# Kernel tuning notes

Measured on AMD Instinct MI355X. Metric: run time of the kernel, lower is better.

## Reference

```python
import jax, jax.numpy as jnp
import numpy as np

EPS = float(jnp.finfo(jnp.float32).eps)


def _mlp(x, W1, b1, W2, b2, W3, b3):
    h = jax.nn.relu(x @ W1 + b1)
    h = jax.nn.relu(h @ W2 + b2)
    return h @ W3 + b3


def setup_inputs() -> dict:
    B, D_A, D_B, K, H = 131072, 16, 16, 32, 256
    key = jax.random.key(0)
    ks = jax.random.split(key, 13)
    def lin(k, fi, fo):
        return jax.random.normal(k, (fi, fo), jnp.float32) * (fi ** -0.5)
    inp = {
        "x": jax.random.uniform(ks[0], (B, D_A + D_B), jnp.float32),
        "hW1": lin(ks[1], D_A, H), "hb1": jnp.zeros((H,), jnp.float32),
        "hW2": lin(ks[2], H, H),   "hb2": jnp.zeros((H,), jnp.float32),
        "hW3": lin(ks[3], H, D_B * (K + 1)), "hb3": jnp.zeros((D_B * (K + 1),), jnp.float32),
        "wW1": lin(ks[4], D_A, H), "wb1": jnp.zeros((H,), jnp.float32),
        "wW2": lin(ks[5], H, H),   "wb2": jnp.zeros((H,), jnp.float32),
        "wW3": lin(ks[6], H, D_B * K), "wb3": jnp.zeros((D_B * K,), jnp.float32),
        "A_dims": jnp.arange(0, 32, 2, dtype=jnp.int32),
        "B_dims": jnp.arange(1, 32, 2, dtype=jnp.int32),
    }
    return inp


def reference(x, hW1, hb1, hW2, hb2, hW3, hb3, wW1, wb1, wW2, wb2, wW3, wb3, A_dims, B_dims):
    B = x.shape[0]
    D_B = B_dims.shape[0]
    K = wW3.shape[1] // D_B
    x_A = x[:, A_dims]               # (B, D_A)
    x_B = x[:, B_dims]               # (B, D_B)

    raw_h = _mlp(x_A, hW1, hb1, hW2, hb2, hW3, hb3).reshape(B, D_B, K + 1)
    heights = jax.nn.softplus(raw_h) + EPS
    raw_w = _mlp(x_A, wW1, wb1, wW2, wb2, wW3, wb3).reshape(B, D_B, K)
    widths = jax.nn.softmax(raw_w, axis=-1)
    zeros = jnp.zeros((B, D_B, 1), x.dtype)
    bins = jnp.concatenate([zeros, jnp.cumsum(widths, axis=-1)], axis=-1)  # (B, D_B, K+1)

    # preprocess_params_2: normalise PDF heights and bin areas
    bin_widths = bins[:, :, 1:] - bins[:, :, :-1]
    bin_areas = 0.5 * (heights[:, :, :-1] + heights[:, :, 1:]) * bin_widths  # (B, D_B, K)
    total_area = bin_areas.sum(axis=-1, keepdims=True)
    v = heights / total_area
    bin_areas = bin_areas / total_area

    # bin search
    i = jnp.sum(x_B[..., None] >= bins, axis=-1) - 1
    i = jnp.clip(i, 0, K - 1)                                  # (B, D_B)
    iu = i[..., None]

    x_left = jnp.take_along_axis(bins, iu, axis=2)[..., 0]
    x_right = jnp.take_along_axis(bins, iu + 1, axis=2)[..., 0]
    w_b = x_right - x_left
    v_left = jnp.take_along_axis(v, iu, axis=2)[..., 0]
    v_right = jnp.take_along_axis(v, iu + 1, axis=2)[..., 0]
    w_v = v_right - v_left

    alpha = (x_B - x_left) / (w_b + EPS)
    # cumulative area up to left edge of bin i: exclusive prefix sum then gather
    c_edges = jnp.concatenate([zeros, jnp.cumsum(bin_areas, axis=-1)], axis=-1)
    c_left = jnp.take_along_axis(c_edges, iu, axis=2)[..., 0]

    y_B = c_left + 0.5 * alpha ** 2 * w_v * w_b + alpha * v_left * w_b
    y = x.at[:, B_dims].set(y_B)
    return y
```

## Files before the change

### kernel.cpp

```cpp
#include <hip/hip_runtime.h>
#include <cmath>

typedef short short8 __attribute__((ext_vector_type(8)));
typedef short short4v __attribute__((ext_vector_type(4)));
typedef float f32x16 __attribute__((ext_vector_type(16)));

#define EPSF 1.1920929e-07f

#define LDS_A2W 0
#define LDS_A2H 16896
#define LDS_A1W 33792
#define LDS_A1H 50688
#define LDS_EW  33792
#define LDS_HH  52224
#define LDS_XA  70656
#define LDS_TOTAL 71680

#define OFF1H 0
#define OFF1W 4096
#define OFF2H 8192
#define OFF2W 73728
#define OFF3H 139264
#define OFF3W 278528

__device__ __forceinline__ unsigned short f2bf(float f) {
  union { float f; unsigned u; } v; v.f = f;
  return (unsigned short)((v.u + 0x8000u) >> 16);
}
__device__ __forceinline__ float bf2f(unsigned short h) {
  union { unsigned u; float f; } v; v.u = ((unsigned)h) << 16; return v.f;
}

__global__ void pack_weights(const float* __restrict__ hW1, const float* __restrict__ wW1,
                             const float* __restrict__ hW2, const float* __restrict__ wW2,
                             const float* __restrict__ hW3, const float* __restrict__ wW3,
                             unsigned short* __restrict__ out) {
  int tile = blockIdx.x, l = threadIdx.x;
  const float* src; unsigned short* dst; int NT, N, K, base;
  if (tile < 8)        { src = hW1; dst = out + OFF1H; NT = 8;  N = 256; K = 16;  base = tile; }
  else if (tile < 16)  { src = wW1; dst = out + OFF1W; NT = 8;  N = 256; K = 16;  base = tile - 8; }
  else if (tile < 144) { src = hW2; dst = out + OFF2H; NT = 8;  N = 256; K = 256; base = tile - 16; }
  else if (tile < 272) { src = wW2; dst = out + OFF2W; NT = 8;  N = 256; K = 256; base = tile - 144; }
  else if (tile < 544) { src = hW3; dst = out + OFF3H; NT = 17; N = 528; K = 256; base = tile - 272; }
  else                 { src = wW3; dst = out + OFF3W; NT = 16; N = 512; K = 256; base = tile - 544; }
  int nt = base % NT, kt = base / NT, KTT = K / 16;
  int n = nt * 32 + (l & 31);
  int k0 = kt * 16 + (l >> 5) * 8;
  short8 v;
  #pragma unroll
  for (int e = 0; e < 8; e++) {
    float f = (n < N && (k0 + e) < K) ? src[(k0 + e) * N + n] : 0.f;
    v[e] = (short)f2bf(f);
  }
  int idx = nt * KTT + kt;
  *(short8*)(dst + (idx * 64 + l) * 8) = v;
}

template <int KT>
__device__ __forceinline__ f32x16 gemm_tile(const unsigned short* __restrict__ A, int apitch,
                                            const unsigned short* __restrict__ pB, int ct,
                                            float init) {
  int l = threadIdx.x & 63;
  f32x16 acc;
  #pragma unroll
  for (int r = 0; r < 16; r++) acc[r] = init;
  const unsigned short* aptr = A + (l & 31) * apitch + (l >> 5) * 8;
  const unsigned short* bptr = pB + (ct * KT * 64 + l) * 8;
  #pragma unroll
  for (int kt = 0; kt < KT; kt++) {
    short8 b = *(const short8*)(bptr + kt * 512);
    short8 a = *(const short8*)(aptr + kt * 16);
    acc = __builtin_amdgcn_mfma_f32_32x32x16_bf16(a, b, acc, 0, 0, 0);
  }
  return acc;
}

__device__ __forceinline__ void epi_relu(char* lds, int oOff, f32x16 acc, int ct) {
  int l = threadIdx.x & 63;
  int col = ct * 32 + (l & 31);
  unsigned short* o = (unsigned short*)(lds + oOff) + col + 4 * (l >> 5) * 264;
  #pragma unroll
  for (int r = 0; r < 16; r++) {
    int row = (r & 3) + 8 * (r >> 2);
    o[row * 264] = f2bf(fmaxf(acc[r], 0.f));
  }
}

__global__ __launch_bounds__(512, 4) void fused_kernel(
    const float* __restrict__ x,
    const float* __restrict__ hb1, const float* __restrict__ hb2, const float* __restrict__ hb3,
    const float* __restrict__ wb1, const float* __restrict__ wb2, const float* __restrict__ wb3,
    const unsigned short* __restrict__ pw,
    float* __restrict__ y) {
  extern __shared__ char lds[];
  const int t = threadIdx.x;
  const int w = t >> 6, l = t & 63;
  const int r0 = blockIdx.x * 32;

  if (t < 256) {
    int row = t >> 3, c4 = t & 7;
    float4 v = *(const float4*)(x + (r0 + row) * 32 + c4 * 4);
    y[(r0 + row) * 32 + c4 * 4] = v.x;
    y[(r0 + row) * 32 + c4 * 4 + 2] = v.z;
    unsigned short* xa = (unsigned short*)(lds + LDS_XA) + row * 16 + c4 * 2;
    xa[0] = f2bf(v.x); xa[1] = f2bf(v.z);
  }
  __syncthreads();

  const unsigned short* XA  = (const unsigned short*)(lds + LDS_XA);
  const unsigned short* A1W = (const unsigned short*)(lds + LDS_A1W);
  const unsigned short* A1H = (const unsigned short*)(lds + LDS_A1H);
  const unsigned short* A2W = (const unsigned short*)(lds + LDS_A2W);
  const unsigned short* A2H = (const unsigned short*)(lds + LDS_A2H);
  const int colw = w * 32 + (l & 31);

  { f32x16 aw = gemm_tile<1>(XA, 16, pw + OFF1W, w, wb1[colw]);
    epi_relu(lds, LDS_A1W, aw, w);
    f32x16 ah = gemm_tile<1>(XA, 16, pw + OFF1H, w, hb1[colw]);
    epi_relu(lds, LDS_A1H, ah, w); }
  __syncthreads();
  { f32x16 aw = gemm_tile<16>(A1W, 264, pw + OFF2W, w, wb2[colw]);
    epi_relu(lds, LDS_A2W, aw, w);
    f32x16 ah = gemm_tile<16>(A1H, 264, pw + OFF2H, w, hb2[colw]);
    epi_relu(lds, LDS_A2H, ah, w); }
  __syncthreads();

  #pragma unroll 1
  for (int H = 0; H < 2; H++) {
    for (int u = w; u < 17; u += 8) {
      int rbase = 4 * (l >> 5);
      if (u < 8) {
        int ctg = H * 8 + u;
        f32x16 a = gemm_tile<16>(A2W, 264, pw + OFF3W, ctg, wb3[ctg * 32 + (l & 31)]);
        unsigned short* o = (unsigned short*)(lds + LDS_EW) + rbase * 288 + (ctg & 7) * 36 + (l & 31);
        #pragma unroll
        for (int r = 0; r < 16; r++) {
          int row = (r & 3) + 8 * (r >> 2);
          o[row * 288] = f2bf(__expf(a[r]));
        }
      } else {
        int ctg = (u - 8) + 8 * H;
        int c = ctg * 32 + (l & 31);
        float bv = (c < 528) ? hb3[c] : 0.f;
        f32x16 a = gemm_tile<16>(A2H, 264, pw + OFF3H, ctg, bv);
        if (c >= 264 * H && c < 264 * (H + 1)) {
          unsigned d = ((unsigned)c * 993u) >> 15;
          int j = c - 33 * (int)d;
          unsigned short* o = (unsigned short*)(lds + LDS_HH) + rbase * 288 + ((int)d & 7) * 36 + j;
          #pragma unroll
          for (int r = 0; r < 16; r++) {
            int row = (r & 3) + 8 * (r >> 2);
            float v = a[r];
            float sp = fmaxf(v, 0.f) + __logf(1.f + __expf(-fabsf(v))) + EPSF;
            o[row * 288] = f2bf(sp);
          }
        }
      }
    }
    __syncthreads();

    {
      int p = t >> 1, half = t & 1;
      int row = p >> 3, dl = p & 7, dg = H * 8 + dl;
      const unsigned short* EWb = (const unsigned short*)(lds + LDS_EW) + row * 288 + dl * 36;
      const unsigned short* HHb = (const unsigned short*)(lds + LDS_HH) + row * 288 + dl * 36;
      const unsigned short* EWp = EWb + half * 16;
      const unsigned short* HHp = HHb + half * 16;
      float e[16], hh[17];
      #pragma unroll
      for (int i = 0; i < 4; i++) {
        short4v ev = *(const short4v*)(EWp + i * 4);
        short4v hv = *(const short4v*)(HHp + i * 4);
        #pragma unroll
        for (int jj = 0; jj < 4; jj++) {
          e[i * 4 + jj] = bf2f((unsigned short)ev[jj]);
          hh[i * 4 + jj] = bf2f((unsigned short)hv[jj]);
        }
      }
      hh[16] = bf2f(HHp[16]);
      float se = 0.f;
      #pragma unroll
      for (int k = 0; k < 16; k++) se += e[k];
      float so = __shfl_xor(se, 1);
      float s = se + so;
      float xbv = x[(r0 + row) * 32 + 2 * dg + 1];
      float xbs = xbv * s;
      float bl0 = half ? so : 0.f;
      int fnd = (xbs >= bl0) ? 1 : 0;
      float bl = bl0, cl2 = 0.f, sxl = bl0, scl2 = 0.f;
      int ki = 0;
      #pragma unroll
      for (int k = 0; k < 16; k++) {
        bool c = (xbs >= bl);
        ki   = c ? k   : ki;
        sxl  = c ? bl  : sxl;
        scl2 = c ? cl2 : scl2;
        cl2 += (hh[k] + hh[k + 1]) * e[k];
        bl  += e[k];
      }
      float cl2o = __shfl_xor(cl2, 1);
      float S2 = cl2 + cl2o;
      if (half) scl2 += cl2o;
      int   o_ki   = __shfl_xor(ki, 1);
      float o_sxl  = __shfl_xor(sxl, 1);
      float o_scl2 = __shfl_xor(scl2, 1);
      int   o_fnd  = __shfl_xor(fnd, 1);
      bool other = half ? (fnd == 0) : (o_fnd != 0);
      int   gki   = other ? o_ki   : ki;
      int   ghalf = other ? (half ^ 1) : half;
      float gsxl  = other ? o_sxl  : sxl;
      float gscl2 = other ? o_scl2 : scl2;
      int go = ghalf * 16 + gki;
      float sew = bf2f(EWb[go]);
      float shl = bf2f(HHb[go]);
      float shr = bf2f(HHb[go + 1]);
      float alpha = (xbs - gsxl) / (sew + EPSF);
      float yv = (gscl2 + (alpha * alpha * (shr - shl) + 2.f * alpha * shl) * sew) / S2;
      if (!half) y[(r0 + row) * 32 + 2 * dg + 1] = yv;
    }
    __syncthreads();
  }
}

extern "C" void kernel_launch(void* const* d_in, const int* in_sizes, int n_in,
                              void* d_out, int out_size, void* d_ws, size_t ws_size,
                              hipStream_t stream) {
  const float* x   = (const float*)d_in[0];
  const float* hW1 = (const float*)d_in[1];
  const float* hb1 = (const float*)d_in[2];
  const float* hW2 = (const float*)d_in[3];
  const float* hb2 = (const float*)d_in[4];
  const float* hW3 = (const float*)d_in[5];
  const float* hb3 = (const float*)d_in[6];
  const float* wW1 = (const float*)d_in[7];
  const float* wb1 = (const float*)d_in[8];
  const float* wW2 = (const float*)d_in[9];
  const float* wb2 = (const float*)d_in[10];
  const float* wW3 = (const float*)d_in[11];
  const float* wb3 = (const float*)d_in[12];
  unsigned short* pw = (unsigned short*)d_ws;

  pack_weights<<<800, 64, 0, stream>>>(hW1, wW1, hW2, wW2, hW3, wW3, pw);

  hipFuncSetAttribute((const void*)fused_kernel,
                      hipFuncAttributeMaxDynamicSharedMemorySize, LDS_TOTAL);
  fused_kernel<<<4096, 512, LDS_TOTAL, stream>>>(
      x, hb1, hb2, hb3, wb1, wb2, wb3, pw, (float*)d_out);
}
```

Baseline: 201.2 us.

## Double rows per block so each weight fragment feeds two MFMA tiles

Each block now processes 64 rows with 1024 threads instead of 32 rows with 512. Every wave issues two 32x32 MFMAs per loaded weight fragment, which halves the global/L2 weight traffic per row. Layer-1 and layer-2 work is split between waves 0-7 (width net) and 8-15 (height net) instead of having each wave do both. In exchange, the LDS footprint roughly doubles to about 141KB, which likely limits residency to one block per CU, and the 17th output tile of layer 3 lands on a single wave, which may cause load imbalance.

New measurement: 190.5 us. -5.3%, faster.

```diff
diff --git a/kernel.cpp b/kernel.cpp
--- a/kernel.cpp
+++ b/kernel.cpp
@@ -8,13 +8,13 @@
 #define EPSF 1.1920929e-07f
 
 #define LDS_A2W 0
-#define LDS_A2H 16896
-#define LDS_A1W 33792
-#define LDS_A1H 50688
-#define LDS_EW  33792
-#define LDS_HH  52224
-#define LDS_XA  70656
-#define LDS_TOTAL 71680
+#define LDS_A2H 33792
+#define LDS_A1W 67584
+#define LDS_A1H 101376
+#define LDS_XA  135168
+#define LDS_EW  67584
+#define LDS_HH  104448
+#define LDS_TOTAL 141312
 
 #define OFF1H 0
 #define OFF1W 4096
@@ -56,37 +56,43 @@
   *(short8*)(dst + (idx * 64 + l) * 8) = v;
 }
 
+struct Acc2 { f32x16 a0, a1; };
+
 template <int KT>
-__device__ __forceinline__ f32x16 gemm_tile(const unsigned short* __restrict__ A, int apitch,
-                                            const unsigned short* __restrict__ pB, int ct,
-                                            float init) {
+__device__ __forceinline__ Acc2 gemm_tile2(const unsigned short* __restrict__ A, int apitch,
+                                           const unsigned short* __restrict__ pB, int ct,
+                                           float init) {
   int l = threadIdx.x & 63;
-  f32x16 acc;
-  #pragma unroll
-  for (int r = 0; r < 16; r++) acc[r] = init;
-  const unsigned short* aptr = A + (l & 31) * apitch + (l >> 5) * 8;
+  Acc2 r;
+  #pragma unroll
+  for (int i = 0; i < 16; i++) { r.a0[i] = init; r.a1[i] = init; }
+  const unsigned short* aptr0 = A + (l & 31) * apitch + (l >> 5) * 8;
+  const unsigned short* aptr1 = aptr0 + 32 * apitch;
   const unsigned short* bptr = pB + (ct * KT * 64 + l) * 8;
   #pragma unroll
   for (int kt = 0; kt < KT; kt++) {
     short8 b = *(const short8*)(bptr + kt * 512);
-    short8 a = *(const short8*)(aptr + kt * 16);
-    acc = __builtin_amdgcn_mfma_f32_32x32x16_bf16(a, b, acc, 0, 0, 0);
-  }
-  return acc;
-}
-
-__device__ __forceinline__ void epi_relu(char* lds, int oOff, f32x16 acc, int ct) {
+    short8 a0 = *(const short8*)(aptr0 + kt * 16);
+    short8 a1 = *(const short8*)(aptr1 + kt * 16);
+    r.a0 = __builtin_amdgcn_mfma_f32_32x32x16_bf16(a0, b, r.a0, 0, 0, 0);
+    r.a1 = __builtin_amdgcn_mfma_f32_32x32x16_bf16(a1, b, r.a1, 0, 0, 0);
+  }
+  return r;
+}
+
+__device__ __forceinline__ void epi_relu2(char* lds, int oOff, Acc2 a, int ct) {
   int l = threadIdx.x & 63;
   int col = ct * 32 + (l & 31);
   unsigned short* o = (unsigned short*)(lds + oOff) + col + 4 * (l >> 5) * 264;
   #pragma unroll
   for (int r = 0; r < 16; r++) {
     int row = (r & 3) + 8 * (r >> 2);
-    o[row * 264] = f2bf(fmaxf(acc[r], 0.f));
-  }
-}
-
-__global__ __launch_bounds__(512, 4) void fused_kernel(
+    o[row * 264] = f2bf(fmaxf(a.a0[r], 0.f));
+    o[(row + 32) * 264] = f2bf(fmaxf(a.a1[r], 0.f));
+  }
+}
+
+__global__ __launch_bounds__(1024, 4) void fused_kernel(
     const float* __restrict__ x,
     const float* __restrict__ hb1, const float* __restrict__ hb2, const float* __restrict__ hb3,
     const float* __restrict__ wb1, const float* __restrict__ wb2, const float* __restrict__ wb3,
@@ -95,9 +101,9 @@
   extern __shared__ char lds[];
   const int t = threadIdx.x;
   const int w = t >> 6, l = t & 63;
-  const int r0 = blockIdx.x * 32;
-
-  if (t < 256) {
+  const int r0 = blockIdx.x * 64;
+
+  if (t < 512) {
     int row = t >> 3, c4 = t & 7;
     float4 v = *(const float4*)(x + (r0 + row) * 32 + c4 * 4);
     y[(r0 + row) * 32 + c4 * 4] = v.x;
@@ -112,47 +118,47 @@
   const unsigned short* A1H = (const unsigned short*)(lds + LDS_A1H);
   const unsigned short* A2W = (const unsigned short*)(lds + LDS_A2W);
   const unsigned short* A2H = (const unsigned short*)(lds + LDS_A2H);
-  const int colw = w * 32 + (l & 31);
-
-  { f32x16 aw = gemm_tile<1>(XA, 16, pw + OFF1W, w, wb1[colw]);
-    epi_relu(lds, LDS_A1W, aw, w);
-    f32x16 ah = gemm_tile<1>(XA, 16, pw + OFF1H, w, hb1[colw]);
-    epi_relu(lds, LDS_A1H, ah, w); }
+  const int ct8 = w & 7;
+  const int col8 = ct8 * 32 + (l & 31);
+
+  if (w < 8) { epi_relu2(lds, LDS_A1W, gemm_tile2<1>(XA, 16, pw + OFF1W, ct8, wb1[col8]), ct8); }
+  else       { epi_relu2(lds, LDS_A1H, gemm_tile2<1>(XA, 16, pw + OFF1H, ct8, hb1[col8]), ct8); }
   __syncthreads();
-  { f32x16 aw = gemm_tile<16>(A1W, 264, pw + OFF2W, w, wb2[colw]);
-    epi_relu(lds, LDS_A2W, aw, w);
-    f32x16 ah = gemm_tile<16>(A1H, 264, pw + OFF2H, w, hb2[colw]);
-    epi_relu(lds, LDS_A2H, ah, w); }
+  if (w < 8) { epi_relu2(lds, LDS_A2W, gemm_tile2<16>(A1W, 264, pw + OFF2W, ct8, wb2[col8]), ct8); }
+  else       { epi_relu2(lds, LDS_A2H, gemm_tile2<16>(A1H, 264, pw + OFF2H, ct8, hb2[col8]), ct8); }
   __syncthreads();
 
   #pragma unroll 1
   for (int H = 0; H < 2; H++) {
-    for (int u = w; u < 17; u += 8) {
-      int rbase = 4 * (l >> 5);
+    for (int u = w; u < 17; u += 16) {
       if (u < 8) {
         int ctg = H * 8 + u;
-        f32x16 a = gemm_tile<16>(A2W, 264, pw + OFF3W, ctg, wb3[ctg * 32 + (l & 31)]);
-        unsigned short* o = (unsigned short*)(lds + LDS_EW) + rbase * 288 + (ctg & 7) * 36 + (l & 31);
+        Acc2 a = gemm_tile2<16>(A2W, 264, pw + OFF3W, ctg, wb3[ctg * 32 + (l & 31)]);
+        unsigned short* o = (unsigned short*)(lds + LDS_EW) + (ctg & 7) * 36 + (l & 31)
+                            + 4 * (l >> 5) * 288;
         #pragma unroll
         for (int r = 0; r < 16; r++) {
           int row = (r & 3) + 8 * (r >> 2);
-          o[row * 288] = f2bf(__expf(a[r]));
+          o[row * 288] = f2bf(__expf(a.a0[r]));
+          o[(row + 32) * 288] = f2bf(__expf(a.a1[r]));
         }
       } else {
         int ctg = (u - 8) + 8 * H;
         int c = ctg * 32 + (l & 31);
         float bv = (c < 528) ? hb3[c] : 0.f;
-        f32x16 a = gemm_tile<16>(A2H, 264, pw + OFF3H, ctg, bv);
+        Acc2 a = gemm_tile2<16>(A2H, 264, pw + OFF3H, ctg, bv);
         if (c >= 264 * H && c < 264 * (H + 1)) {
           unsigned d = ((unsigned)c * 993u) >> 15;
           int j = c - 33 * (int)d;
-          unsigned short* o = (unsigned short*)(lds + LDS_HH) + rbase * 288 + ((int)d & 7) * 36 + j;
+          unsigned short* o = (unsigned short*)(lds + LDS_HH) + ((int)d & 7) * 36 + j
+                              + 4 * (l >> 5) * 288;
           #pragma unroll
           for (int r = 0; r < 16; r++) {
             int row = (r & 3) + 8 * (r >> 2);
-            float v = a[r];
-            float sp = fmaxf(v, 0.f) + __logf(1.f + __expf(-fabsf(v))) + EPSF;
-            o[row * 288] = f2bf(sp);
+            float v0 = a.a0[r];
+            o[row * 288] = f2bf(fmaxf(v0, 0.f) + __logf(1.f + __expf(-fabsf(v0))) + EPSF);
+            float v1 = a.a1[r];
+            o[(row + 32) * 288] = f2bf(fmaxf(v1, 0.f) + __logf(1.f + __expf(-fabsf(v1))) + EPSF);
           }
         }
       }
@@ -244,6 +250,6 @@
 
   hipFuncSetAttribute((const void*)fused_kernel,
                       hipFuncAttributeMaxDynamicSharedMemorySize, LDS_TOTAL);
-  fused_kernel<<<4096, 512, LDS_TOTAL, stream>>>(
+  fused_kernel<<<2048, 1024, LDS_TOTAL, stream>>>(
       x, hb1, hb2, hb3, wb1, wb2, wb3, pw, (float*)d_out);
 }
```
